# Kernel tuning notes

Hardware: AMD Instinct MI355X
Metric: run time of the kernel (lower is better)

Reference implementation:

```python
import jax, jax.numpy as jnp
import numpy as np

B, T, D, H, O, E = 2, 2048, 1024, 4096, 1024, 8


def setup_inputs() -> dict:
    key = jax.random.key(0)
    ks = jax.random.split(key, 8)
    s = lambda fan_in: 1.0 / np.sqrt(fan_in)
    return {
        "x": jax.random.normal(ks[0], (B, T, D), dtype=jnp.float32),
        "Wg": jax.random.uniform(ks[1], (D, E), minval=-s(D), maxval=s(D)),
        "bg": jax.random.uniform(ks[2], (E,), minval=-s(D), maxval=s(D)),
        "W1": jax.random.uniform(ks[3], (E, D, H), minval=-s(D), maxval=s(D)),
        "b1": jax.random.uniform(ks[4], (E, H), minval=-s(D), maxval=s(D)),
        "W2": jax.random.uniform(ks[5], (E, H, O), minval=-s(H), maxval=s(H)),
        "b2": jax.random.uniform(ks[6], (E, O), minval=-s(H), maxval=s(H)),
        "num_experts_per_tok": 2,
    }


def reference(x, Wg, bg, W1, b1, W2, b2, num_experts_per_tok):
    # gating: softmax over experts  [B,T,E]
    scores = jax.nn.softmax(jnp.einsum('btd,de->bte', x, Wg) + bg, axis=-1)
    # top-k mask (scatter of ones at topk indices)
    _, idx = jax.lax.top_k(scores, num_experts_per_tok)          # [B,T,k]
    mask = jax.nn.one_hot(idx, E, dtype=scores.dtype).sum(axis=-2)  # [B,T,E]
    gated = scores * mask
    # F.normalize(p=1): divide by L1 norm clamped to eps
    gated = gated / jnp.maximum(jnp.sum(jnp.abs(gated), axis=-1, keepdims=True), 1e-12)
    # all experts run on all tokens (naive MoE)
    hidden = jax.nn.relu(jnp.einsum('btd,edh->beth', x, W1) + b1[None, :, None, :])  # [B,E,T,H]
    expert_out = jnp.einsum('beth,eho->beto', hidden, W2) + b2[None, :, None, :]     # [B,E,T,O]
    # combine: einsum('bte,bteo->bto') with expert_outputs transposed(1,2)
    return jnp.einsum('bte,beto->bto', gated, expert_out)
```

## Files before the change

kernel.cpp:

```cpp
#include <hip/hip_runtime.h>
#include <hip/hip_bf16.h>
#include <cstdio>

#define NT_TOK 4096
#define D_DIM  1024
#define H_DIM  4096
#define O_DIM  1024
#define E_NUM  8
#define PAIRS  8192
#define WI_SLOTS 72
#define BK 64

typedef short bf16x8 __attribute__((ext_vector_type(8)));
typedef float f32x4  __attribute__((ext_vector_type(4)));

__device__ __forceinline__ unsigned short bfr(float f){
  unsigned u = __float_as_uint(f);
  unsigned r = (u + 0x7FFFu + ((u >> 16) & 1u)) >> 16;
  return (unsigned short)r;
}

__device__ __forceinline__ void gload_lds16(const void* g, void* l){
  __builtin_amdgcn_global_load_lds((const __attribute__((address_space(1))) unsigned int*)g,
                                   (__attribute__((address_space(3))) unsigned int*)l,
                                   16, 0, 0);
}

__global__ __launch_bounds__(256) void transpose_cast64(const float* __restrict__ in,
                                                        unsigned short* __restrict__ out,
                                                        int R, int C){
  __shared__ float t[64][65];
  long long base = (long long)blockIdx.z * R * C;
  int c0 = blockIdx.x * 64, r0 = blockIdx.y * 64;
  int tid = threadIdx.x;
  int rr = tid >> 4;
  int cc = (tid & 15) * 4;
  #pragma unroll
  for (int i = 0; i < 4; i++){
    int r = rr + i * 16;
    float4 v = *(const float4*)&in[base + (long long)(r0 + r) * C + c0 + cc];
    t[r][cc] = v.x; t[r][cc+1] = v.y; t[r][cc+2] = v.z; t[r][cc+3] = v.w;
  }
  __syncthreads();
  #pragma unroll
  for (int i = 0; i < 4; i++){
    int oc = rr + i * 16;
    unsigned int lo = (unsigned int)bfr(t[cc][oc])   | ((unsigned int)bfr(t[cc+1][oc]) << 16);
    unsigned int hi = (unsigned int)bfr(t[cc+2][oc]) | ((unsigned int)bfr(t[cc+3][oc]) << 16);
    *(uint2*)&out[base + (long long)(c0 + oc) * R + r0 + cc] = make_uint2(lo, hi);
  }
}

__global__ __launch_bounds__(256) void gating_kernel(const float* __restrict__ x,
                                                     const float* __restrict__ Wg,
                                                     const float* __restrict__ bg,
                                                     unsigned short* __restrict__ xb,
                                                     int*   __restrict__ pe,
                                                     float* __restrict__ pw){
  int wid = threadIdx.x >> 6, lane = threadIdx.x & 63;
  int t = blockIdx.x * 4 + wid;
  const float* xr = x + (long long)t * D_DIM;
  unsigned short* xo = xb + (long long)t * D_DIM;
  float acc[E_NUM];
  #pragma unroll
  for (int e = 0; e < E_NUM; e++) acc[e] = 0.f;
  for (int d = lane; d < D_DIM; d += 64){
    float xv = xr[d];
    xo[d] = bfr(xv);
    const float* wr = Wg + d * E_NUM;
    #pragma unroll
    for (int e = 0; e < E_NUM; e++) acc[e] += xv * wr[e];
  }
  #pragma unroll
  for (int off = 32; off; off >>= 1)
    #pragma unroll
    for (int e = 0; e < E_NUM; e++) acc[e] += __shfl_xor(acc[e], off);
  if (lane == 0){
    float l[E_NUM];
    float m = -1e30f;
    #pragma unroll
    for (int e = 0; e < E_NUM; e++){ l[e] = acc[e] + bg[e]; m = fmaxf(m, l[e]); }
    float ex[E_NUM];
    #pragma unroll
    for (int e = 0; e < E_NUM; e++) ex[e] = expf(l[e] - m);
    int e0 = 0;
    #pragma unroll
    for (int e = 1; e < E_NUM; e++) if (ex[e] > ex[e0]) e0 = e;
    int e1 = -1;
    for (int e = 0; e < E_NUM; e++){ if (e == e0) continue; if (e1 < 0 || ex[e] > ex[e1]) e1 = e; }
    float s = ex[e0] + ex[e1];
    pe[2*t]   = e0;  pw[2*t]   = ex[e0] / s;
    pe[2*t+1] = e1;  pw[2*t+1] = ex[e1] / s;
  }
}

__global__ __launch_bounds__(256) void hist_kernel(const int* __restrict__ pe,
                                                   int* __restrict__ chunk_hist){
  __shared__ int h[E_NUM];
  if (threadIdx.x < E_NUM) h[threadIdx.x] = 0;
  __syncthreads();
  int p = blockIdx.x * 256 + threadIdx.x;
  atomicAdd(&h[pe[p]], 1);
  __syncthreads();
  if (threadIdx.x < E_NUM) chunk_hist[blockIdx.x * E_NUM + threadIdx.x] = h[threadIdx.x];
}

__global__ __launch_bounds__(256) void scatter_kernel(const int* __restrict__ pe,
                                                      const int* __restrict__ chunk_hist,
                                                      int* __restrict__ cnt,
                                                      int* __restrict__ offs,
                                                      int* __restrict__ row_pair,
                                                      int* __restrict__ wi){
  __shared__ int hist[32][E_NUM];
  __shared__ int pref[32][E_NUM];
  __shared__ int total[E_NUM];
  __shared__ int off_s[E_NUM + 1];
  __shared__ unsigned char ex[PAIRS];
  int tid = threadIdx.x;
  for (int i = tid; i < PAIRS; i += 256) ex[i] = (unsigned char)pe[i];
  { int c = tid >> 3, e = tid & 7; hist[c][e] = chunk_hist[tid]; }
  __syncthreads();
  if (tid < E_NUM){
    int s = 0;
    for (int c = 0; c < 32; c++){ pref[c][tid] = s; s += hist[c][tid]; }
    total[tid] = s;
  }
  __syncthreads();
  if (tid == 0){
    int s = 0;
    for (int e = 0; e < E_NUM; e++){ off_s[e] = s; s += total[e]; }
    off_s[E_NUM] = s;
    int idx = 0;
    for (int e = 0; e < E_NUM; e++){
      int mts = (total[e] + 127) >> 7;
      for (int m = 0; m < mts; m++) wi[idx++] = (e << 8) | m;
    }
    for (; idx < WI_SLOTS; idx++) wi[idx] = -1;
  }
  __syncthreads();
  if (tid < E_NUM){ cnt[tid] = total[tid]; offs[tid] = off_s[tid]; }
  int c = tid >> 3, e = tid & 7;
  int base = off_s[e] + pref[c][e];
  int local = 0;
  for (int i = 0; i < 256; i++){
    int p = c * 256 + i;
    if (ex[p] == (unsigned char)e){
      row_pair[base + local] = p;
      local++;
    }
  }
}

__global__ __launch_bounds__(256, 3) void gemm1_kernel(const unsigned short* __restrict__ xb,
                                                       const unsigned short* __restrict__ W1t,
                                                       const float* __restrict__ b1,
                                                       const int* __restrict__ row_pair,
                                                       const int* __restrict__ cnt,
                                                       const int* __restrict__ offs,
                                                       const int* __restrict__ wi,
                                                       unsigned short* __restrict__ hidden){
  int w = wi[blockIdx.y];
  if (w < 0) return;
  int e = w >> 8, mt = w & 255;
  int nt = blockIdx.x;
  int count = cnt[e];
  int m0 = mt * 128;
  int seg = offs[e];
  int valid = count - m0;
  int n0 = nt * 128;

  __shared__ unsigned short As[128 * BK];
  __shared__ unsigned short Bs[128 * BK];

  int tid = threadIdx.x;
  int wv = tid >> 6, lane = tid & 63;
  int wr = wv >> 1, wc = wv & 1;
  int lo = lane & 15, hi = lane >> 4;
  int l3 = lane >> 3;
  int srcel = ((lane & 7) ^ l3) << 3;

  const unsigned short* w1e = W1t + (long long)e * H_DIM * D_DIM;

  const unsigned short* pa[4];
  const unsigned short* pb[4];
  #pragma unroll
  for (int h = 0; h < 4; h++){
    int r = h * 32 + wv * 8 + l3;
    int pos = seg + m0 + r; if (pos > PAIRS - 1) pos = PAIRS - 1;
    int token = row_pair[pos] >> 1;
    pa[h] = xb + (long long)token * D_DIM + srcel;
    pb[h] = w1e + (long long)(n0 + r) * D_DIM + srcel;
  }

  f32x4 acc[4][4] = {};
  for (int kt = 0; kt < D_DIM / BK; ++kt){
    #pragma unroll
    for (int h = 0; h < 4; h++){
      gload_lds16(pa[h], &As[(h*32 + wv*8) * BK]);  pa[h] += BK;
      gload_lds16(pb[h], &Bs[(h*32 + wv*8) * BK]);  pb[h] += BK;
    }
    __syncthreads();
    bf16x8 aq[4][2], bq[4][2];
    #pragma unroll
    for (int n = 0; n < 4; n++)
      #pragma unroll
      for (int ks = 0; ks < 2; ks++){
        int br = wc*64 + n*16 + lo;
        bq[n][ks] = *(const bf16x8*)&Bs[br*BK + ((ks*32 + hi*8) ^ ((br & 7) << 3))];
      }
    #pragma unroll
    for (int m = 0; m < 4; m++)
      #pragma unroll
      for (int ks = 0; ks < 2; ks++){
        int ar = wr*64 + m*16 + lo;
        aq[m][ks] = *(const bf16x8*)&As[ar*BK + ((ks*32 + hi*8) ^ ((ar & 7) << 3))];
      }
    #pragma unroll
    for (int m = 0; m < 4; m++)
      #pragma unroll
      for (int n = 0; n < 4; n++)
        #pragma unroll
        for (int ks = 0; ks < 2; ks++)
          acc[m][n] = __builtin_amdgcn_mfma_f32_16x16x32_bf16(aq[m][ks], bq[n][ks], acc[m][n], 0, 0, 0);
    __syncthreads();
  }

  const float* b1e = b1 + (long long)e * H_DIM;
  #pragma unroll
  for (int n = 0; n < 4; n++){
    int col = n0 + wc*64 + n*16 + lo;
    float bias = b1e[col];
    #pragma unroll
    for (int m = 0; m < 4; m++)
      #pragma unroll
      for (int j = 0; j < 4; j++){
        int rl = wr*64 + m*16 + hi*4 + j;
        if (rl < valid){
          float v = acc[m][n][j] + bias;
          v = v > 0.f ? v : 0.f;
          hidden[(long long)(seg + m0 + rl) * H_DIM + col] = bfr(v);
        }
      }
  }
}

__global__ __launch_bounds__(256, 3) void gemm2_kernel(const unsigned short* __restrict__ hidden,
                                                       const unsigned short* __restrict__ W2t,
                                                       const int* __restrict__ row_pair,
                                                       const int* __restrict__ cnt,
                                                       const int* __restrict__ offs,
                                                       const int* __restrict__ wi,
                                                       float* __restrict__ yp){
  int w = wi[blockIdx.y];
  if (w < 0) return;
  int e = w >> 8, mt = w & 255;
  int nt = blockIdx.x;
  int kpart = blockIdx.z;
  int count = cnt[e];
  int m0 = mt * 128;
  int seg = offs[e];
  int valid = count - m0;
  int n0 = nt * 128;
  int k0 = kpart * (H_DIM / 2);
  float* y = yp + (long long)kpart * PAIRS * O_DIM;

  __shared__ unsigned short As[128 * BK];
  __shared__ unsigned short Bs[128 * BK];

  int tid = threadIdx.x;
  int wv = tid >> 6, lane = tid & 63;
  int wr = wv >> 1, wc = wv & 1;
  int lo = lane & 15, hi = lane >> 4;
  int l3 = lane >> 3;
  int srcel = ((lane & 7) ^ l3) << 3;

  const unsigned short* w2e = W2t + (long long)e * O_DIM * H_DIM;

  const unsigned short* pa[4];
  const unsigned short* pb[4];
  #pragma unroll
  for (int h = 0; h < 4; h++){
    int r = h * 32 + wv * 8 + l3;
    long long pos = seg + m0 + r; if (pos > PAIRS - 1) pos = PAIRS - 1;
    pa[h] = hidden + pos * H_DIM + k0 + srcel;
    pb[h] = w2e + (long long)(n0 + r) * H_DIM + k0 + srcel;
  }

  f32x4 acc[4][4] = {};
  for (int kt = 0; kt < (H_DIM / 2) / BK; ++kt){
    #pragma unroll
    for (int h = 0; h < 4; h++){
      gload_lds16(pa[h], &As[(h*32 + wv*8) * BK]);  pa[h] += BK;
      gload_lds16(pb[h], &Bs[(h*32 + wv*8) * BK]);  pb[h] += BK;
    }
    __syncthreads();
    bf16x8 aq[4][2], bq[4][2];
    #pragma unroll
    for (int n = 0; n < 4; n++)
      #pragma unroll
      for (int ks = 0; ks < 2; ks++){
        int br = wc*64 + n*16 + lo;
        bq[n][ks] = *(const bf16x8*)&Bs[br*BK + ((ks*32 + hi*8) ^ ((br & 7) << 3))];
      }
    #pragma unroll
    for (int m = 0; m < 4; m++)
      #pragma unroll
      for (int ks = 0; ks < 2; ks++){
        int ar = wr*64 + m*16 + lo;
        aq[m][ks] = *(const bf16x8*)&As[ar*BK + ((ks*32 + hi*8) ^ ((ar & 7) << 3))];
      }
    #pragma unroll
    for (int m = 0; m < 4; m++)
      #pragma unroll
      for (int n = 0; n < 4; n++)
        #pragma unroll
        for (int ks = 0; ks < 2; ks++)
          acc[m][n] = __builtin_amdgcn_mfma_f32_16x16x32_bf16(aq[m][ks], bq[n][ks], acc[m][n], 0, 0, 0);
    __syncthreads();
  }

  #pragma unroll
  for (int m = 0; m < 4; m++)
    #pragma unroll
    for (int j = 0; j < 4; j++){
      int rl = wr*64 + m*16 + hi*4 + j;
      if (rl < valid){
        int p = row_pair[seg + m0 + rl];
        float* yr = y + (long long)p * O_DIM;
        #pragma unroll
        for (int n = 0; n < 4; n++){
          int col = n0 + wc*64 + n*16 + lo;
          yr[col] = acc[m][n][j];
        }
      }
    }
}

__global__ __launch_bounds__(256) void combine_kernel(const float* __restrict__ yp,
                                                      const float* __restrict__ b2,
                                                      const int* __restrict__ pe,
                                                      const float* __restrict__ pw,
                                                      float* __restrict__ out){
  int t = blockIdx.x, tid = threadIdx.x;
  int e0 = pe[2*t], e1 = pe[2*t+1];
  float w0 = pw[2*t], w1 = pw[2*t+1];
  const float* y0 = yp;
  const float* y1 = yp + (long long)PAIRS * O_DIM;
  float4 a0 = ((const float4*)(y0 + (long long)(2*t) * O_DIM))[tid];
  float4 a1 = ((const float4*)(y1 + (long long)(2*t) * O_DIM))[tid];
  float4 b0 = ((const float4*)(y0 + (long long)(2*t+1) * O_DIM))[tid];
  float4 b1 = ((const float4*)(y1 + (long long)(2*t+1) * O_DIM))[tid];
  float4 ca = ((const float4*)(b2 + (long long)e0 * O_DIM))[tid];
  float4 cb = ((const float4*)(b2 + (long long)e1 * O_DIM))[tid];
  float4 r;
  r.x = w0 * (a0.x + a1.x + ca.x) + w1 * (b0.x + b1.x + cb.x);
  r.y = w0 * (a0.y + a1.y + ca.y) + w1 * (b0.y + b1.y + cb.y);
  r.z = w0 * (a0.z + a1.z + ca.z) + w1 * (b0.z + b1.z + cb.z);
  r.w = w0 * (a0.w + a1.w + ca.w) + w1 * (b0.w + b1.w + cb.w);
  ((float4*)(out + (long long)t * O_DIM))[tid] = r;
}

extern "C" void kernel_launch(void* const* d_in, const int* in_sizes, int n_in,
                              void* d_out, int out_size, void* d_ws, size_t ws_size,
                              hipStream_t stream){
  const float* x  = (const float*)d_in[0];
  const float* Wg = (const float*)d_in[1];
  const float* bg = (const float*)d_in[2];
  const float* W1 = (const float*)d_in[3];
  const float* b1 = (const float*)d_in[4];
  const float* W2 = (const float*)d_in[5];
  const float* b2 = (const float*)d_in[6];
  float* out = (float*)d_out;

  char* ws = (char*)d_ws;
  size_t off = 0;
  auto alloc = [&](size_t bytes){ size_t r = off; off += (bytes + 255) & ~(size_t)255; return r; };

  unsigned short* W1t    = (unsigned short*)(ws + alloc((size_t)E_NUM * H_DIM * D_DIM * 2));
  unsigned short* W2t    = (unsigned short*)(ws + alloc((size_t)E_NUM * O_DIM * H_DIM * 2));
  unsigned short* xb     = (unsigned short*)(ws + alloc((size_t)NT_TOK * D_DIM * 2));
  unsigned short* hidden = (unsigned short*)(ws + alloc((size_t)PAIRS * H_DIM * 2));
  int*            pe     = (int*)           (ws + alloc(PAIRS * 4));
  float*          pw     = (float*)         (ws + alloc(PAIRS * 4));
  int*            row_pair = (int*)         (ws + alloc(PAIRS * 4));
  int*            cnt    = (int*)           (ws + alloc(64));
  int*            offs   = (int*)           (ws + alloc(64));
  int*            chist  = (int*)           (ws + alloc(32 * E_NUM * 4));
  int*            wi     = (int*)           (ws + alloc(WI_SLOTS * 4));

  float* yp = (float*)W1t;

  if (off > ws_size)
    fprintf(stderr, "kernel_launch: workspace too small: need %zu, have %zu\n", off, ws_size);

  transpose_cast64<<<dim3(H_DIM/64, D_DIM/64, E_NUM), 256, 0, stream>>>(W1, W1t, D_DIM, H_DIM);
  transpose_cast64<<<dim3(O_DIM/64, H_DIM/64, E_NUM), 256, 0, stream>>>(W2, W2t, H_DIM, O_DIM);
  gating_kernel<<<NT_TOK/4, 256, 0, stream>>>(x, Wg, bg, xb, pe, pw);
  hist_kernel<<<PAIRS/256, 256, 0, stream>>>(pe, chist);
  scatter_kernel<<<1, 256, 0, stream>>>(pe, chist, cnt, offs, row_pair, wi);
  gemm1_kernel<<<dim3(H_DIM/128, WI_SLOTS), 256, 0, stream>>>(xb, W1t, b1, row_pair, cnt, offs, wi, hidden);
  gemm2_kernel<<<dim3(O_DIM/128, WI_SLOTS, 2), 256, 0, stream>>>(hidden, W2t, row_pair, cnt, offs, wi, yp);
  combine_kernel<<<NT_TOK, 256, 0, stream>>>(yp, b2, pe, pw, out);
}
```

Baseline: 339.1 us.

## Fuse weight transposes into gating and gemm1 launches, drop split-K in gemm2

The W1 transpose/cast now runs as extra blocks in the gating kernel, and the W2 transpose runs as extra blocks appended to the gemm1 grid, so the independent work overlaps and fewer launches are needed. The histogram kernel is removed in favour of global atomics from gating after a memset. gemm2 no longer splits K in two: each block runs the full K loop and adds b2 itself, so combine reads half as much data. The cost is that gemm2 now has half as many blocks, each with a longer serial K loop, which may underfill the GPU.

```diff
diff --git a/kernel.cpp b/kernel.cpp
--- a/kernel.cpp
+++ b/kernel.cpp
@@ -10,6 +10,9 @@
 #define PAIRS  8192
 #define WI_SLOTS 72
 #define BK 64
+#define G1_BLOCKS (32 * WI_SLOTS)
+#define TW1_BLOCKS (E_NUM * 1024)
+#define TW2_BLOCKS (E_NUM * 1024)
 
 typedef short bf16x8 __attribute__((ext_vector_type(8)));
 typedef float f32x4  __attribute__((ext_vector_type(4)));
@@ -26,12 +29,13 @@
                                    16, 0, 0);
 }
 
-__global__ __launch_bounds__(256) void transpose_cast64(const float* __restrict__ in,
-                                                        unsigned short* __restrict__ out,
-                                                        int R, int C){
-  __shared__ float t[64][65];
-  long long base = (long long)blockIdx.z * R * C;
-  int c0 = blockIdx.x * 64, r0 = blockIdx.y * 64;
+__device__ __forceinline__ void transpose_tile(const float* __restrict__ in,
+                                               unsigned short* __restrict__ out,
+                                               int R, int C, int bx, int by, int bz,
+                                               char* smem){
+  float (*t)[65] = (float(*)[65])smem;
+  long long base = (long long)bz * R * C;
+  int c0 = bx * 64, r0 = by * 64;
   int tid = threadIdx.x;
   int rr = tid >> 4;
   int cc = (tid & 15) * 4;
@@ -51,14 +55,25 @@
   }
 }
 
-__global__ __launch_bounds__(256) void gating_kernel(const float* __restrict__ x,
-                                                     const float* __restrict__ Wg,
-                                                     const float* __restrict__ bg,
-                                                     unsigned short* __restrict__ xb,
-                                                     int*   __restrict__ pe,
-                                                     float* __restrict__ pw){
+__global__ __launch_bounds__(256) void gate_w1t_kernel(const float* __restrict__ x,
+                                                       const float* __restrict__ Wg,
+                                                       const float* __restrict__ bg,
+                                                       const float* __restrict__ W1,
+                                                       unsigned short* __restrict__ xb,
+                                                       unsigned short* __restrict__ W1t,
+                                                       int*   __restrict__ pe,
+                                                       float* __restrict__ pw,
+                                                       int*   __restrict__ chist){
+  __shared__ __align__(16) char smem[16640];
+  int bid = blockIdx.x;
+  if (bid >= NT_TOK/4){
+    int tb = bid - NT_TOK/4;
+    int e = tb >> 10, t = tb & 1023;
+    transpose_tile(W1, W1t, D_DIM, H_DIM, t & 63, t >> 6, e, smem);
+    return;
+  }
   int wid = threadIdx.x >> 6, lane = threadIdx.x & 63;
-  int t = blockIdx.x * 4 + wid;
+  int t = bid * 4 + wid;
   const float* xr = x + (long long)t * D_DIM;
   unsigned short* xo = xb + (long long)t * D_DIM;
   float acc[E_NUM];
@@ -91,18 +106,10 @@
     float s = ex[e0] + ex[e1];
     pe[2*t]   = e0;  pw[2*t]   = ex[e0] / s;
     pe[2*t+1] = e1;  pw[2*t+1] = ex[e1] / s;
-  }
-}
-
-__global__ __launch_bounds__(256) void hist_kernel(const int* __restrict__ pe,
-                                                   int* __restrict__ chunk_hist){
-  __shared__ int h[E_NUM];
-  if (threadIdx.x < E_NUM) h[threadIdx.x] = 0;
-  __syncthreads();
-  int p = blockIdx.x * 256 + threadIdx.x;
-  atomicAdd(&h[pe[p]], 1);
-  __syncthreads();
-  if (threadIdx.x < E_NUM) chunk_hist[blockIdx.x * E_NUM + threadIdx.x] = h[threadIdx.x];
+    int chunk = (2*t) >> 8;
+    atomicAdd(&chist[chunk * E_NUM + e0], 1);
+    atomicAdd(&chist[chunk * E_NUM + e1], 1);
+  }
 }
 
 __global__ __launch_bounds__(256) void scatter_kernel(const int* __restrict__ pe,
@@ -151,14 +158,117 @@
   }
 }
 
-__global__ __launch_bounds__(256, 3) void gemm1_kernel(const unsigned short* __restrict__ xb,
-                                                       const unsigned short* __restrict__ W1t,
-                                                       const float* __restrict__ b1,
+__global__ __launch_bounds__(256, 3) void gemm1_w2t_kernel(const unsigned short* __restrict__ xb,
+                                                           const unsigned short* __restrict__ W1t,
+                                                           const float* __restrict__ W2,
+                                                           unsigned short* __restrict__ W2t,
+                                                           const float* __restrict__ b1,
+                                                           const int* __restrict__ row_pair,
+                                                           const int* __restrict__ cnt,
+                                                           const int* __restrict__ offs,
+                                                           const int* __restrict__ wi,
+                                                           unsigned short* __restrict__ hidden){
+  __shared__ __align__(16) char smem[32768];
+  int bid = blockIdx.x;
+  if (bid >= G1_BLOCKS){
+    int tb = bid - G1_BLOCKS;
+    int e = tb >> 10, t = tb & 1023;
+    transpose_tile(W2, W2t, H_DIM, O_DIM, t & 15, t >> 4, e, smem);
+    return;
+  }
+  int nt = bid & 31, slot = bid >> 5;
+  int w = wi[slot];
+  if (w < 0) return;
+  int e = w >> 8, mt = w & 255;
+  int count = cnt[e];
+  int m0 = mt * 128;
+  int seg = offs[e];
+  int valid = count - m0;
+  int n0 = nt * 128;
+
+  unsigned short* As = (unsigned short*)smem;
+  unsigned short* Bs = (unsigned short*)(smem + 16384);
+
+  int tid = threadIdx.x;
+  int wv = tid >> 6, lane = tid & 63;
+  int wr = wv >> 1, wc = wv & 1;
+  int lo = lane & 15, hi = lane >> 4;
+  int l3 = lane >> 3;
+  int srcel = ((lane & 7) ^ l3) << 3;
+
+  const unsigned short* w1e = W1t + (long long)e * H_DIM * D_DIM;
+
+  const unsigned short* pa[4];
+  const unsigned short* pb[4];
+  #pragma unroll
+  for (int h = 0; h < 4; h++){
+    int r = h * 32 + wv * 8 + l3;
+    int pos = seg + m0 + r; if (pos > PAIRS - 1) pos = PAIRS - 1;
+    int token = row_pair[pos] >> 1;
+    pa[h] = xb + (long long)token * D_DIM + srcel;
+    pb[h] = w1e + (long long)(n0 + r) * D_DIM + srcel;
+  }
+
+  f32x4 acc[4][4] = {};
+  for (int kt = 0; kt < D_DIM / BK; ++kt){
+    #pragma unroll
+    for (int h = 0; h < 4; h++){
+      gload_lds16(pa[h], &As[(h*32 + wv*8) * BK]);  pa[h] += BK;
+      gload_lds16(pb[h], &Bs[(h*32 + wv*8) * BK]);  pb[h] += BK;
+    }
+    __syncthreads();
+    bf16x8 aq[4][2], bq[4][2];
+    #pragma unroll
+    for (int n = 0; n < 4; n++)
+      #pragma unroll
+      for (int ks = 0; ks < 2; ks++){
+        int br = wc*64 + n*16 + lo;
+        bq[n][ks] = *(const bf16x8*)&Bs[br*BK + ((ks*32 + hi*8) ^ ((br & 7) << 3))];
+      }
+    #pragma unroll
+    for (int m = 0; m < 4; m++)
+      #pragma unroll
+      for (int ks = 0; ks < 2; ks++){
+        int ar = wr*64 + m*16 + lo;
+        aq[m][ks] = *(const bf16x8*)&As[ar*BK + ((ks*32 + hi*8) ^ ((ar & 7) << 3))];
+      }
+    #pragma unroll
+    for (int m = 0; m < 4; m++)
+      #pragma unroll
+      for (int n = 0; n < 4; n++)
+        #pragma unroll
+        for (int ks = 0; ks < 2; ks++)
+          acc[m][n] = __builtin_amdgcn_mfma_f32_16x16x32_bf16(aq[m][ks], bq[n][ks], acc[m][n], 0, 0, 0);
+    __syncthreads();
+  }
+
+  const float* b1e = b1 + (long long)e * H_DIM;
+  #pragma unroll
+  for (int n = 0; n < 4; n++){
+    int col = n0 + wc*64 + n*16 + lo;
+    float bias = b1e[col];
+    #pragma unroll
+    for (int m = 0; m < 4; m++)
+      #pragma unroll
+      for (int j = 0; j < 4; j++){
+        int rl = wr*64 + m*16 + hi*4 + j;
+        if (rl < valid){
+          float v = acc[m][n][j] + bias;
+          v = v > 0.f ? v : 0.f;
+          hidden[(long long)(seg + m0 + rl) * H_DIM + col] = bfr(v);
+        }
+      }
+  }
+}
+
+__global__ __launch_bounds__(256, 3) void gemm2_kernel(const unsigned short* __restrict__ hidden,
+                                                       const unsigned short* __restrict__ W2t,
+                                                       const float* __restrict__ b2,
                                                        const int* __restrict__ row_pair,
                                                        const int* __restrict__ cnt,
                                                        const int* __restrict__ offs,
                                                        const int* __restrict__ wi,
-                                                       unsigned short* __restrict__ hidden){
+                                                       float* __restrict__ y){
   int w = wi[blockIdx.y];
   if (w < 0) return;
   int e = w >> 8, mt = w & 255;
@@ -179,21 +289,20 @@
   int l3 = lane >> 3;
   int srcel = ((lane & 7) ^ l3) << 3;
 
-  const unsigned short* w1e = W1t + (long long)e * H_DIM * D_DIM;
+  const unsigned short* w2e = W2t + (long long)e * O_DIM * H_DIM;
 
   const unsigned short* pa[4];
   const unsigned short* pb[4];
   #pragma unroll
   for (int h = 0; h < 4; h++){
     int r = h * 32 + wv * 8 + l3;
-    int pos = seg + m0 + r; if (pos > PAIRS - 1) pos = PAIRS - 1;
-    int token = row_pair[pos] >> 1;
-    pa[h] = xb + (long long)token * D_DIM + srcel;
-    pb[h] = w1e + (long long)(n0 + r) * D_DIM + srcel;
+    long long pos = seg + m0 + r; if (pos > PAIRS - 1) pos = PAIRS - 1;
+    pa[h] = hidden + pos * H_DIM + srcel;
+    pb[h] = w2e + (long long)(n0 + r) * H_DIM + srcel;
   }
 
   f32x4 acc[4][4] = {};
-  for (int kt = 0; kt < D_DIM / BK; ++kt){
+  for (int kt = 0; kt < H_DIM / BK; ++kt){
     #pragma unroll
     for (int h = 0; h < 4; h++){
       gload_lds16(pa[h], &As[(h*32 + wv*8) * BK]);  pa[h] += BK;
@@ -225,100 +334,7 @@
     __syncthreads();
   }
 
-  const float* b1e = b1 + (long long)e * H_DIM;
-  #pragma unroll
-  for (int n = 0; n < 4; n++){
-    int col = n0 + wc*64 + n*16 + lo;
-    float bias = b1e[col];
-    #pragma unroll
-    for (int m = 0; m < 4; m++)
-      #pragma unroll
-      for (int j = 0; j < 4; j++){
-        int rl = wr*64 + m*16 + hi*4 + j;
-        if (rl < valid){
-          float v = acc[m][n][j] + bias;
-          v = v > 0.f ? v : 0.f;
-          hidden[(long long)(seg + m0 + rl) * H_DIM + col] = bfr(v);
-        }
-      }
-  }
-}
-
-__global__ __launch_bounds__(256, 3) void gemm2_kernel(const unsigned short* __restrict__ hidden,
-                                                       const unsigned short* __restrict__ W2t,
-                                                       const int* __restrict__ row_pair,
-                                                       const int* __restrict__ cnt,
-                                                       const int* __restrict__ offs,
-                                                       const int* __restrict__ wi,
-                                                       float* __restrict__ yp){
-  int w = wi[blockIdx.y];
-  if (w < 0) return;
-  int e = w >> 8, mt = w & 255;
-  int nt = blockIdx.x;
-  int kpart = blockIdx.z;
-  int count = cnt[e];
-  int m0 = mt * 128;
-  int seg = offs[e];
-  int valid = count - m0;
-  int n0 = nt * 128;
-  int k0 = kpart * (H_DIM / 2);
-  float* y = yp + (long long)kpart * PAIRS * O_DIM;
-
-  __shared__ unsigned short As[128 * BK];
-  __shared__ unsigned short Bs[128 * BK];
-
-  int tid = threadIdx.x;
-  int wv = tid >> 6, lane = tid & 63;
-  int wr = wv >> 1, wc = wv & 1;
-  int lo = lane & 15, hi = lane >> 4;
-  int l3 = lane >> 3;
-  int srcel = ((lane & 7) ^ l3) << 3;
-
-  const unsigned short* w2e = W2t + (long long)e * O_DIM * H_DIM;
-
-  const unsigned short* pa[4];
-  const unsigned short* pb[4];
-  #pragma unroll
-  for (int h = 0; h < 4; h++){
-    int r = h * 32 + wv * 8 + l3;
-    long long pos = seg + m0 + r; if (pos > PAIRS - 1) pos = PAIRS - 1;
-    pa[h] = hidden + pos * H_DIM + k0 + srcel;
-    pb[h] = w2e + (long long)(n0 + r) * H_DIM + k0 + srcel;
-  }
-
-  f32x4 acc[4][4] = {};
-  for (int kt = 0; kt < (H_DIM / 2) / BK; ++kt){
-    #pragma unroll
-    for (int h = 0; h < 4; h++){
-      gload_lds16(pa[h], &As[(h*32 + wv*8) * BK]);  pa[h] += BK;
-      gload_lds16(pb[h], &Bs[(h*32 + wv*8) * BK]);  pb[h] += BK;
-    }
-    __syncthreads();
-    bf16x8 aq[4][2], bq[4][2];
-    #pragma unroll
-    for (int n = 0; n < 4; n++)
-      #pragma unroll
-      for (int ks = 0; ks < 2; ks++){
-        int br = wc*64 + n*16 + lo;
-        bq[n][ks] = *(const bf16x8*)&Bs[br*BK + ((ks*32 + hi*8) ^ ((br & 7) << 3))];
-      }
-    #pragma unroll
-    for (int m = 0; m < 4; m++)
-      #pragma unroll
-      for (int ks = 0; ks < 2; ks++){
-        int ar = wr*64 + m*16 + lo;
-        aq[m][ks] = *(const bf16x8*)&As[ar*BK + ((ks*32 + hi*8) ^ ((ar & 7) << 3))];
-      }
-    #pragma unroll
-    for (int m = 0; m < 4; m++)
-      #pragma unroll
-      for (int n = 0; n < 4; n++)
-        #pragma unroll
-        for (int ks = 0; ks < 2; ks++)
-          acc[m][n] = __builtin_amdgcn_mfma_f32_16x16x32_bf16(aq[m][ks], bq[n][ks], acc[m][n], 0, 0, 0);
-    __syncthreads();
-  }
-
+  const float* b2e = b2 + (long long)e * O_DIM;
   #pragma unroll
   for (int m = 0; m < 4; m++)
     #pragma unroll
@@ -330,33 +346,25 @@
         #pragma unroll
         for (int n = 0; n < 4; n++){
           int col = n0 + wc*64 + n*16 + lo;
-          yr[col] = acc[m][n][j];
+          yr[col] = acc[m][n][j] + b2e[col];
         }
       }
     }
 }
 
-__global__ __launch_bounds__(256) void combine_kernel(const float* __restrict__ yp,
-                                                      const float* __restrict__ b2,
+__global__ __launch_bounds__(256) void combine_kernel(const float* __restrict__ y,
                                                       const int* __restrict__ pe,
                                                       const float* __restrict__ pw,
                                                       float* __restrict__ out){
   int t = blockIdx.x, tid = threadIdx.x;
-  int e0 = pe[2*t], e1 = pe[2*t+1];
   float w0 = pw[2*t], w1 = pw[2*t+1];
-  const float* y0 = yp;
-  const float* y1 = yp + (long long)PAIRS * O_DIM;
-  float4 a0 = ((const float4*)(y0 + (long long)(2*t) * O_DIM))[tid];
-  float4 a1 = ((const float4*)(y1 + (long long)(2*t) * O_DIM))[tid];
-  float4 b0 = ((const float4*)(y0 + (long long)(2*t+1) * O_DIM))[tid];
-  float4 b1 = ((const float4*)(y1 + (long long)(2*t+1) * O_DIM))[tid];
-  float4 ca = ((const float4*)(b2 + (long long)e0 * O_DIM))[tid];
-  float4 cb = ((const float4*)(b2 + (long long)e1 * O_DIM))[tid];
+  float4 a = ((const float4*)(y + (long long)(2*t) * O_DIM))[tid];
+  float4 b = ((const float4*)(y + (long long)(2*t+1) * O_DIM))[tid];
   float4 r;
-  r.x = w0 * (a0.x + a1.x + ca.x) + w1 * (b0.x + b1.x + cb.x);
-  r.y = w0 * (a0.y + a1.y + ca.y) + w1 * (b0.y + b1.y + cb.y);
-  r.z = w0 * (a0.z + a1.z + ca.z) + w1 * (b0.z + b1.z + cb.z);
-  r.w = w0 * (a0.w + a1.w + ca.w) + w1 * (b0.w + b1.w + cb.w);
+  r.x = w0 * a.x + w1 * b.x;
+  r.y = w0 * a.y + w1 * b.y;
+  r.z = w0 * a.z + w1 * b.z;
+  r.w = w0 * a.w + w1 * b.w;
   ((float4*)(out + (long long)t * O_DIM))[tid] = r;
 }
 
@@ -393,12 +401,11 @@
   if (off > ws_size)
     fprintf(stderr, "kernel_launch: workspace too small: need %zu, have %zu\n", off, ws_size);
 
-  transpose_cast64<<<dim3(H_DIM/64, D_DIM/64, E_NUM), 256, 0, stream>>>(W1, W1t, D_DIM, H_DIM);
-  transpose_cast64<<<dim3(O_DIM/64, H_DIM/64, E_NUM), 256, 0, stream>>>(W2, W2t, H_DIM, O_DIM);
-  gating_kernel<<<NT_TOK/4, 256, 0, stream>>>(x, Wg, bg, xb, pe, pw);
-  hist_kernel<<<PAIRS/256, 256, 0, stream>>>(pe, chist);
+  hipMemsetAsync(chist, 0, 32 * E_NUM * 4, stream);
+  gate_w1t_kernel<<<NT_TOK/4 + TW1_BLOCKS, 256, 0, stream>>>(x, Wg, bg, W1, xb, W1t, pe, pw, chist);
   scatter_kernel<<<1, 256, 0, stream>>>(pe, chist, cnt, offs, row_pair, wi);
-  gemm1_kernel<<<dim3(H_DIM/128, WI_SLOTS), 256, 0, stream>>>(xb, W1t, b1, row_pair, cnt, offs, wi, hidden);
-  gemm2_kernel<<<dim3(O_DIM/128, WI_SLOTS, 2), 256, 0, stream>>>(hidden, W2t, row_pair, cnt, offs, wi, yp);
-  combine_kernel<<<NT_TOK, 256, 0, stream>>>(yp, b2, pe, pw, out);
-}
+  gemm1_w2t_kernel<<<G1_BLOCKS + TW2_BLOCKS, 256, 0, stream>>>(xb, W1t, W2, W2t, b1,
+                                                               row_pair, cnt, offs, wi, hidden);
+  gemm2_kernel<<<dim3(O_DIM/128, WI_SLOTS), 256, 0, stream>>>(hidden, W2t, b2, row_pair, cnt, offs, wi, yp);
+  combine_kernel<<<NT_TOK, 256, 0, stream>>>(yp, pe, pw, out);
+}
```

Result: faster. 324.0 us (-4.4%).
